# Performance work log

Hardware: AMD Instinct MI355X
Metric: run time of the kernel (lower is better)

The kernel has to match this reference:

```python
import jax, jax.numpy as jnp
import numpy as np

FEAT, HID, HEADS, OUT, NLAYERS = 32, 64, 6, 1, 4
NG, NP, K = 16, 1000, 10
EPS_BN, EPS_IN = 1e-5, 1e-5


def _build_graph(pos, rng=None):
    # knn_graph(k=10, loop=True, batch=batch) -> to_undirected -> add_self_loops
    N = NG * NP
    parts = []
    for g in range(NG):
        off = g * NP
        p = pos[off:off + NP]
        d2 = ((p[:, None, :] - p[None, :, :]) ** 2).sum(-1)
        nbr = np.argsort(d2, axis=1)[:, :K] + off  # includes self (loop=True)
        src = nbr.reshape(-1)
        dst = np.repeat(np.arange(NP) + off, K)
        parts.append(np.stack([src, dst]))
    ei = np.concatenate(parts, axis=1)
    und = np.unique(np.concatenate([ei, ei[::-1]], axis=1).T, axis=0).T  # to_undirected (coalesced)
    loops = np.tile(np.arange(N), (2, 1))  # add_self_loops (PyG appends unconditionally)
    return np.concatenate([und, loops], axis=1).astype(np.int64)


def setup_inputs() -> dict:
    rng = np.random.default_rng(0)
    N = NG * NP
    pos = rng.standard_normal((N, 3)).astype(np.float32)
    batch = np.repeat(np.arange(NG), NP).astype(np.int64)
    edge_index = _build_graph(pos)

    def lin(fi, fo):
        return (rng.standard_normal((fi, fo)) / np.sqrt(fi)).astype(np.float32)

    HC = HEADS * HID
    z = lambda *s: jnp.zeros(s, jnp.float32)
    o = lambda *s: jnp.ones(s, jnp.float32)
    return dict(
        x=jnp.asarray(rng.standard_normal((N, FEAT)).astype(np.float32)),
        pos=jnp.asarray(pos),
        w_lin1=jnp.asarray(lin(FEAT, HID)), b_lin1=z(HID),
        w_e1=jnp.asarray(lin(1, 32)), b_e1=z(32),
        w_e2=jnp.asarray(lin(32, 1)), b_e2=z(1),
        Wl=jnp.asarray(np.stack([lin(HID, HC) for _ in range(NLAYERS)])), bl=z(NLAYERS, HC),
        Wr=jnp.asarray(np.stack([lin(HID, HC) for _ in range(NLAYERS)])), br=z(NLAYERS, HC),
        We=jnp.asarray(np.stack([lin(1, HC) for _ in range(NLAYERS)])),
        att=jnp.asarray((rng.standard_normal((NLAYERS, HEADS, HID)) / np.sqrt(HID)).astype(np.float32)),
        b_gat=z(NLAYERS, HID),
        w_emb1=jnp.asarray(lin(HID, HID)), b_emb1=z(HID),
        bn1_g=o(HID), bn1_b=z(HID), bn1_m=z(HID), bn1_v=o(HID),
        w_emb2=jnp.asarray(lin(HID, HID)), b_emb2=z(HID),
        bn2_g=o(HID), bn2_b=z(HID), bn2_m=z(HID), bn2_v=o(HID),
        w_pred=jnp.asarray(lin(HID, OUT)), b_pred=z(OUT),
        edge_index=jnp.asarray(edge_index),
        batch=jnp.asarray(batch),
        n_graphs=NG,
    )


def _bn_eval(x, g, b, m, v):
    return (x - m) / jnp.sqrt(v + EPS_BN) * g + b


def _inorm(h, batch, n_graphs):
    # PyG InstanceNorm (affine=False): per-graph, per-channel standardization
    ones = jnp.ones((h.shape[0], 1), h.dtype)
    cnt = jax.ops.segment_sum(ones, batch, num_segments=n_graphs)
    mean = jax.ops.segment_sum(h, batch, num_segments=n_graphs) / cnt
    hc = h - mean[batch]
    var = jax.ops.segment_sum(hc * hc, batch, num_segments=n_graphs) / cnt
    return hc / jnp.sqrt(var[batch] + EPS_IN)


def _gatv2(h, src, dst, ea, Wl, bl, Wr, br, We, att, bias, n):
    # GATv2Conv(heads=HEADS, concat=False, edge_dim=1)
    xl = (h @ Wl + bl).reshape(-1, HEADS, HID)  # [N,H,C] source proj
    xr = (h @ Wr + br).reshape(-1, HEADS, HID)  # [N,H,C] target proj
    e = (ea @ We).reshape(-1, HEADS, HID)       # [E,H,C] edge proj (bias=False)
    g = jax.nn.leaky_relu(xl[src] + xr[dst] + e, 0.2)
    alpha = jnp.einsum('ehc,hc->eh', g, att)    # [E,H]
    amax = jax.ops.segment_max(alpha, dst, num_segments=n)
    ex = jnp.exp(alpha - amax[dst])
    den = jax.ops.segment_sum(ex, dst, num_segments=n)
    a = ex / (den[dst] + 1e-16)                 # PyG softmax eps
    out = jax.ops.segment_sum(xl[src] * a[:, :, None], dst, num_segments=n)
    return out.mean(axis=1) + bias              # concat=False -> head mean


def reference(x, pos, w_lin1, b_lin1, w_e1, b_e1, w_e2, b_e2, Wl, bl, Wr, br, We, att, b_gat,
              w_emb1, b_emb1, bn1_g, bn1_b, bn1_m, bn1_v, w_emb2, b_emb2,
              bn2_g, bn2_b, bn2_m, bn2_v, w_pred, b_pred, edge_index, batch, n_graphs):
    src, dst = edge_index[0], edge_index[1]
    d = pos[src] - pos[dst]
    s = (d * d).sum(-1, keepdims=True)
    ew = jnp.where(s == 0, 0.0, jnp.sqrt(jnp.where(s == 0, 1.0, s)))  # safe norm (0-grad at 0)
    m = jax.nn.relu(ew @ w_e1 + b_e1)            # MLP([1,32,1]) (BN in eval = identity)
    ea = jax.nn.relu(m @ w_e2 + b_e2)            # relu(edge_MLP(.)) -> [E,1]
    h = x @ w_lin1 + b_lin1
    n = h.shape[0]
    for i in range(NLAYERS):
        h = jax.nn.relu(h + _gatv2(h, src, dst, ea, Wl[i], bl[i], Wr[i], br[i], We[i], att[i], b_gat[i], n))
        h = _inorm(h, batch, n_graphs)
    z = jax.nn.relu(h @ w_emb1 + b_emb1)
    z = _bn_eval(z, bn1_g, bn1_b, bn1_m, bn1_v)
    h_out = z @ w_emb2 + b_emb2
    pred = _bn_eval(h_out, bn2_g, bn2_b, bn2_m, bn2_v) @ w_pred + b_pred
    return h_out, pred
```

## Files before the change

kernel.cpp:

```cpp
#include <hip/hip_runtime.h>
#include <hip/hip_bf16.h>
#include <stdint.h>

typedef __hip_bfloat16 bf16;
typedef __attribute__((ext_vector_type(8))) short short8;
typedef __attribute__((ext_vector_type(4))) float float4v;
__device__ __forceinline__ float bf(const bf16 x){ return __bfloat162float(x); }
__device__ __forceinline__ float bfu(uint32_t u){ u <<= 16; return __uint_as_float(u); }
__device__ __forceinline__ short f2bs(float v){
    bf16 b = __float2bfloat16(v);
    return *(short*)&b;
}

#define FEAT    32
#define HID     64
#define HEADS   6
#define HC      384
#define NLAYERS 4
#define NG      16
#define NP      1000
#define NN      16000
#define EPS_BN  1e-5f
#define EPS_IN  1e-5f
#define MNODE   16
#define LOG2E   1.44269504f
#define STATSZ  (2*NG*HID)
#define NBLK    (NN/4)
#define NTILES  48
#define WPKSZ   (NLAYERS*NTILES*64*16)

__device__ __forceinline__ float normv(float v, const float* st, int g, int c){
    if (!st) return v;
    float s  = st[g*HID + c];
    float s2 = st[NG*HID + g*HID + c];
    float mean = s*(1.f/NP);
    float var  = fmaxf(s2*(1.f/NP) - mean*mean, 0.f);
    return (v - mean)*rsqrtf(var + EPS_IN);
}

__global__ void sentinel_kernel(float* out, int n, float val){
    int i = blockIdx.x*256 + threadIdx.x;
    if (i < n) out[i] = val;
}

__global__ void zero_kernel(int* p, int n){
    int i = blockIdx.x*256 + threadIdx.x;
    if (i < n) p[i] = 0;
}

__global__ void detect_kernel(const int* ei, int* mode){
    __shared__ int nz;
    if (threadIdx.x == 0) nz = 0;
    __syncthreads();
    for (int i = 1 + 2*threadIdx.x; i < 1024; i += 512)
        if (ei[i] != 0) atomicAdd(&nz, 1);
    __syncthreads();
    if (threadIdx.x == 0) *mode = (nz == 0) ? 1 : 0;
}

__device__ __forceinline__ int load_idx(const int* ei, int idx, int mode){
    if (mode) return (int)((const long long*)ei)[idx];
    return ei[idx];
}

__global__ void count_kernel(const int* ei, const int* mode, int* deg, int E){
    int e = blockIdx.x*256 + threadIdx.x;
    if (e >= E) return;
    int d = load_idx(ei, E + e, *mode);
    if (d >= 0 && d < NN) atomicAdd(&deg[d], 1);
}

__global__ void scan_kernel(const int* deg, int* rowptr, int N){
    __shared__ int part[256];
    __shared__ int offs[256];
    int t = threadIdx.x;
    int chunk = (N + 255)/256;
    int lo = t*chunk, hi = lo + chunk; if (hi > N) hi = N;
    int s = 0;
    for (int i = lo; i < hi; i++) s += deg[i];
    part[t] = s;
    __syncthreads();
    if (t == 0){
        int r = 0;
        for (int i = 0; i < 256; i++){ offs[i] = r; r += part[i]; }
        rowptr[N] = r;
    }
    __syncthreads();
    int r = offs[t];
    for (int i = lo; i < hi; i++){ rowptr[i] = r; r += deg[i]; }
}

__global__ void scatter_ea_kernel(const int* ei, const float* pos,
                                  const float* w_e1, const float* b_e1,
                                  const float* w_e2, const float* b_e2,
                                  const int* rowptr, int* fill, const int* mode_p,
                                  int* csr_src, float* ea_csr, int E){
    int e = blockIdx.x*256 + threadIdx.x;
    if (e >= E) return;
    int mode = *mode_p;
    int s = load_idx(ei, e, mode);
    int d = load_idx(ei, E + e, mode);
    if (s < 0 || s >= NN || d < 0 || d >= NN) return;
    float dx = pos[s*3+0] - pos[d*3+0];
    float dy = pos[s*3+1] - pos[d*3+1];
    float dz = pos[s*3+2] - pos[d*3+2];
    float ss = dx*dx + dy*dy + dz*dz;
    float ew = (ss == 0.f) ? 0.f : sqrtf(ss);
    float acc = b_e2[0];
    #pragma unroll
    for (int j = 0; j < 32; j++){
        float m = ew*w_e1[j] + b_e1[j];
        m = m > 0.f ? m : 0.f;
        acc += m*w_e2[j];
    }
    acc = acc > 0.f ? acc : 0.f;
    int p = rowptr[d] + atomicAdd(&fill[d], 1);
    if (p < 0 || p >= E) return;
    csr_src[p] = s;
    ea_csr[p] = acc;
}

__global__ void lin1_kernel(const float* __restrict__ x,
                            const float* __restrict__ w1, const float* __restrict__ b1,
                            float* __restrict__ h, int N){
    int tid = blockIdx.x*256 + threadIdx.x;
    if (tid >= N*HID) return;
    int n = tid >> 6, c = tid & 63;
    float acc = b1[c];
    #pragma unroll
    for (int k = 0; k < FEAT; k++) acc += x[n*FEAT+k] * w1[k*HID+c];
    h[tid] = acc;
}

__global__ void wpack_kernel(const float* __restrict__ Wl,
                             const float* __restrict__ Wr,
                             short* __restrict__ wpk){
    int idx = blockIdx.x*256 + threadIdx.x;
    if (idx >= NLAYERS*NTILES*64) return;
    int layer = idx / (NTILES*64);
    int r = idx - layer*NTILES*64;
    int t = r >> 6, lane = r & 63;
    int q = lane >> 4, m = lane & 15;
    int col = t*16 + m;
    bool isR = col >= HC;
    int c2 = isR ? col - HC : col;
    const float* W = (isR ? Wr : Wl) + (size_t)layer*HID*HC;
    short out[16];
    #pragma unroll
    for (int s = 0; s < 2; s++)
        #pragma unroll
        for (int j = 0; j < 8; j++)
            out[s*8+j] = f2bs(W[(size_t)(s*32 + q*8 + j)*HC + c2]);
    short8* dst = (short8*)(wpk + (size_t)idx*16);
    dst[0] = *(short8*)&out[0];
    dst[1] = *(short8*)&out[8];
}

__global__ __launch_bounds__(256) void xlxr_mfma_kernel(
        const float* __restrict__ h, const float* __restrict__ statPrev,
        const short* __restrict__ wpk,
        const float* __restrict__ bl, const float* __restrict__ br,
        bf16* __restrict__ xl, bf16* __restrict__ xr, int layer){
    int n0 = blockIdx.x*16;
    int wave = threadIdx.x >> 6;
    int lane = threadIdx.x & 63;
    int q = lane >> 4;
    int m = lane & 15;
    int node = n0 + m;
    int g = node / NP;

    short8 afrag[2];
    #pragma unroll
    for (int s = 0; s < 2; s++){
        const float4* hp4 = (const float4*)(h + (size_t)node*HID + s*32 + q*8);
        float4 va = hp4[0], vb = hp4[1];
        int cb = s*32 + q*8;
        afrag[s][0] = f2bs(normv(va.x, statPrev, g, cb+0));
        afrag[s][1] = f2bs(normv(va.y, statPrev, g, cb+1));
        afrag[s][2] = f2bs(normv(va.z, statPrev, g, cb+2));
        afrag[s][3] = f2bs(normv(va.w, statPrev, g, cb+3));
        afrag[s][4] = f2bs(normv(vb.x, statPrev, g, cb+4));
        afrag[s][5] = f2bs(normv(vb.y, statPrev, g, cb+5));
        afrag[s][6] = f2bs(normv(vb.z, statPrev, g, cb+6));
        afrag[s][7] = f2bs(normv(vb.w, statPrev, g, cb+7));
    }

    const float* blp = bl + (size_t)layer*HC;
    const float* brp = br + (size_t)layer*HC;

    for (int t = wave*12; t < wave*12 + 12; t++){
        const short8* bsrc = (const short8*)(wpk + ((size_t)(layer*NTILES + t)*64 + lane)*16);
        short8 b0 = bsrc[0], b1 = bsrc[1];
        float4v acc = {0.f, 0.f, 0.f, 0.f};
        acc = __builtin_amdgcn_mfma_f32_16x16x32_bf16(afrag[0], b0, acc, 0, 0, 0);
        acc = __builtin_amdgcn_mfma_f32_16x16x32_bf16(afrag[1], b1, acc, 0, 0, 0);
        int col = t*16 + m;
        bool isR = col >= HC;
        int c2 = isR ? col - HC : col;
        float bias = isR ? brp[c2] : blp[c2];
        bf16* dst = isR ? xr : xl;
        #pragma unroll
        for (int r = 0; r < 4; r++){
            int row = q*4 + r;
            dst[(size_t)(n0 + row)*HC + c2] = __float2bfloat16(acc[r] + bias);
        }
    }
}

__global__ __launch_bounds__(384) void xlxr_fb_kernel(
        const float* __restrict__ h, const float* __restrict__ statPrev,
        const float* __restrict__ Wl, const float* __restrict__ bl,
        bf16* __restrict__ xl, int layer){
    int n0 = blockIdx.x*MNODE;
    int o = threadIdx.x;
    __shared__ float hh[MNODE*HID];
    for (int i = o; i < MNODE*HID; i += 384){
        int m = i >> 6, k = i & 63;
        int node = n0 + m;
        hh[k*MNODE + m] = normv(h[(size_t)node*HID + k], statPrev, node/NP, k);
    }
    __syncthreads();
    const float* wl = Wl + (size_t)layer*HID*HC;
    float accl[MNODE];
    float bL = bl[layer*HC + o];
    #pragma unroll
    for (int m = 0; m < MNODE; m++) accl[m] = bL;
    for (int k = 0; k < HID; k++){
        float wlv = wl[k*HC + o];
        #pragma unroll
        for (int m = 0; m < MNODE; m++) accl[m] += hh[k*MNODE + m]*wlv;
    }
    #pragma unroll
    for (int m = 0; m < MNODE; m++)
        xl[(size_t)(n0+m)*HC + o] = __float2bfloat16(accl[m]);
}

__global__ __launch_bounds__(256) void agg_kernel(
        const bf16* __restrict__ xl, const bf16* __restrict__ xr,
        const int* __restrict__ rowptr,
        const int* __restrict__ csr_src,
        const float* __restrict__ ea_csr,
        const float* __restrict__ Wr, const float* __restrict__ br,
        const float* __restrict__ We, const float* __restrict__ att,
        const float* __restrict__ b_gat,
        float* __restrict__ h,
        const float* __restrict__ statPrev, float* __restrict__ partial,
        int layer){
    int wave = threadIdx.x >> 6, lane = threadIdx.x & 63;
    int n = blockIdx.x*4 + wave;
    int g = n / NP;
    int r0 = rowptr[n];
    int deg = rowptr[n+1] - r0;

    __shared__ float ps[4][2][HID];

    int grp = lane >> 3, li = lane & 7;
    bool active = grp < HEADS;
    int cb = active ? (grp*HID + li*8) : 0;

    float xrr[8], wer[8], atr[8];
    if (xr){
        if (active){
            const uint4* xru = (const uint4*)(xr + (size_t)n*HC);
            uint4 u = xru[grp*8 + li];
            xrr[0]=bfu(u.x&0xffffu); xrr[1]=bfu(u.x>>16);
            xrr[2]=bfu(u.y&0xffffu); xrr[3]=bfu(u.y>>16);
            xrr[4]=bfu(u.z&0xffffu); xrr[5]=bfu(u.z>>16);
            xrr[6]=bfu(u.w&0xffffu); xrr[7]=bfu(u.w>>16);
        }
    } else {
        float hval = normv(h[(size_t)n*HID + lane], statPrev, g, lane);
        const float* wr = Wr + (size_t)layer*HID*HC;
        #pragma unroll
        for (int i = 0; i < 8; i++) xrr[i] = 0.f;
        for (int k = 0; k < HID; k++){
            float hk = __shfl(hval, k);
            #pragma unroll
            for (int i = 0; i < 8; i++) xrr[i] += hk*wr[k*HC + cb + i];
        }
        #pragma unroll
        for (int i = 0; i < 8; i++) xrr[i] += br[layer*HC + cb + i];
    }
    #pragma unroll
    for (int i = 0; i < 8; i++){
        wer[i] = We[layer*HC + cb + i];
        atr[i] = att[layer*HC + cb + i]*LOG2E;
    }

    float m_ = -1e30f, l_ = 0.f;
    float acc[8];
    #pragma unroll
    for (int i = 0; i < 8; i++) acc[i] = 0.f;

    const uint4* xlu = (const uint4*)xl;

    if (active){
        int j = 0;
        for (; j + 1 < deg; j += 2){
            int sa = csr_src[r0 + j], sb = csr_src[r0 + j + 1];
            float eva = ea_csr[r0 + j], evb = ea_csr[r0 + j + 1];
            uint4 ua = xlu[(size_t)sa*48 + grp*8 + li];
            uint4 ub = xlu[(size_t)sb*48 + grp*8 + li];
            float xa[8], xb[8];
            xa[0]=bfu(ua.x&0xffffu); xa[1]=bfu(ua.x>>16);
            xa[2]=bfu(ua.y&0xffffu); xa[3]=bfu(ua.y>>16);
            xa[4]=bfu(ua.z&0xffffu); xa[5]=bfu(ua.z>>16);
            xa[6]=bfu(ua.w&0xffffu); xa[7]=bfu(ua.w>>16);
            xb[0]=bfu(ub.x&0xffffu); xb[1]=bfu(ub.x>>16);
            xb[2]=bfu(ub.y&0xffffu); xb[3]=bfu(ub.y>>16);
            xb[4]=bfu(ub.z&0xffffu); xb[5]=bfu(ub.z>>16);
            xb[6]=bfu(ub.w&0xffffu); xb[7]=bfu(ub.w>>16);
            float ca = 0.f, cb_ = 0.f;
            #pragma unroll
            for (int i = 0; i < 8; i++){
                float ga = xa[i] + xrr[i] + eva*wer[i];
                ga = fmaxf(ga, 0.2f*ga);
                ca += ga*atr[i];
                float gb = xb[i] + xrr[i] + evb*wer[i];
                gb = fmaxf(gb, 0.2f*gb);
                cb_ += gb*atr[i];
            }
            #pragma unroll
            for (int mm = 1; mm <= 4; mm <<= 1){
                ca  += __shfl_xor(ca, mm);
                cb_ += __shfl_xor(cb_, mm);
            }
            float mn = fmaxf(fmaxf(m_, ca), cb_);
            float r  = exp2f(m_ - mn);
            float pa = exp2f(ca - mn);
            float pb = exp2f(cb_ - mn);
            l_ = l_*r + pa + pb;
            #pragma unroll
            for (int i = 0; i < 8; i++) acc[i] = acc[i]*r + pa*xa[i] + pb*xb[i];
            m_ = mn;
        }
        if (j < deg){
            int sa = csr_src[r0 + j];
            float eva = ea_csr[r0 + j];
            uint4 ua = xlu[(size_t)sa*48 + grp*8 + li];
            float xa[8];
            xa[0]=bfu(ua.x&0xffffu); xa[1]=bfu(ua.x>>16);
            xa[2]=bfu(ua.y&0xffffu); xa[3]=bfu(ua.y>>16);
            xa[4]=bfu(ua.z&0xffffu); xa[5]=bfu(ua.z>>16);
            xa[6]=bfu(ua.w&0xffffu); xa[7]=bfu(ua.w>>16);
            float ca = 0.f;
            #pragma unroll
            for (int i = 0; i < 8; i++){
                float ga = xa[i] + xrr[i] + eva*wer[i];
                ga = fmaxf(ga, 0.2f*ga);
                ca += ga*atr[i];
            }
            #pragma unroll
            for (int mm = 1; mm <= 4; mm <<= 1) ca += __shfl_xor(ca, mm);
            float mn = fmaxf(m_, ca);
            float r  = exp2f(m_ - mn);
            float pa = exp2f(ca - mn);
            l_ = l_*r + pa;
            #pragma unroll
            for (int i = 0; i < 8; i++) acc[i] = acc[i]*r + pa*xa[i];
            m_ = mn;
        }
    }

    float v[8];
    float rl = active ? 1.f/(l_ + 1e-16f) : 0.f;
    #pragma unroll
    for (int i = 0; i < 8; i++) v[i] = acc[i]*rl;
    #pragma unroll
    for (int mm = 8; mm <= 32; mm <<= 1)
        #pragma unroll
        for (int i = 0; i < 8; i++) v[i] += __shfl_xor(v[i], mm);

    if (lane < 8){
        int c0 = lane*8;
        const float4* hp4 = (const float4*)(h + (size_t)n*HID + c0);
        float4 h0 = hp4[0], h1 = hp4[1];
        float hv[8] = {h0.x,h0.y,h0.z,h0.w,h1.x,h1.y,h1.z,h1.w};
        float o[8];
        #pragma unroll
        for (int i = 0; i < 8; i++){
            float r = normv(hv[i], statPrev, g, c0+i)
                    + v[i]*(1.f/HEADS) + b_gat[layer*HID + c0 + i];
            o[i] = r > 0.f ? r : 0.f;
            ps[wave][0][c0+i] = o[i];
            ps[wave][1][c0+i] = o[i]*o[i];
        }
        float4* out4 = (float4*)(h + (size_t)n*HID + c0);
        out4[0] = make_float4(o[0],o[1],o[2],o[3]);
        out4[1] = make_float4(o[4],o[5],o[6],o[7]);
    }
    __syncthreads();
    if (threadIdx.x < HID){
        int c = threadIdx.x;
        float s  = ps[0][0][c] + ps[1][0][c] + ps[2][0][c] + ps[3][0][c];
        float s2 = ps[0][1][c] + ps[1][1][c] + ps[2][1][c] + ps[3][1][c];
        partial[(size_t)blockIdx.x*128 + c]      = s;
        partial[(size_t)blockIdx.x*128 + 64 + c] = s2;
    }
}

__global__ void stat_reduce_kernel(const float* __restrict__ partial,
                                   float* __restrict__ stat){
    int idx = blockIdx.x*256 + threadIdx.x;
    if (idx >= NG*HID) return;
    int g = idx >> 6, c = idx & 63;
    int b0 = g*(NP/4);
    float s = 0.f, s2 = 0.f;
    for (int b = 0; b < NP/4; b++){
        s  += partial[(size_t)(b0+b)*128 + c];
        s2 += partial[(size_t)(b0+b)*128 + 64 + c];
    }
    stat[g*HID + c] = s;
    stat[NG*HID + g*HID + c] = s2;
}

__global__ __launch_bounds__(256) void final_kernel(
        const float* __restrict__ h, const float* __restrict__ statPrev,
        const float* w1, const float* b1,
        const float* g1, const float* be1, const float* m1, const float* v1,
        const float* w2, const float* b2,
        const float* g2, const float* be2, const float* m2, const float* v2,
        const float* wp, const float* bp,
        float* out, int N){
    int wave = threadIdx.x >> 6, c = threadIdx.x & 63;
    int n = blockIdx.x*4 + wave;
    __shared__ float hr[4][HID], zr[4][HID];
    hr[wave][c] = normv(h[(size_t)n*HID + c], statPrev, n/NP, c);
    __syncthreads();
    float z = b1[c];
    #pragma unroll 8
    for (int k = 0; k < HID; k++) z += hr[wave][k]*w1[k*HID+c];
    z = z > 0.f ? z : 0.f;
    z = (z - m1[c]) / sqrtf(v1[c] + EPS_BN) * g1[c] + be1[c];
    zr[wave][c] = z;
    __syncthreads();
    float ho = b2[c];
    #pragma unroll 8
    for (int k = 0; k < HID; k++) ho += zr[wave][k]*w2[k*HID+c];
    out[(size_t)n*HID + c] = ho;
    float t = (ho - m2[c]) / sqrtf(v2[c] + EPS_BN) * g2[c] + be2[c];
    float p = t * wp[c];
    #pragma unroll
    for (int m = 32; m >= 1; m >>= 1) p += __shfl_xor(p, m);
    if (c == 0) out[(size_t)N*HID + n] = p + bp[0];
}

extern "C" void kernel_launch(void* const* d_in, const int* in_sizes, int n_in,
                              void* d_out, int out_size, void* d_ws, size_t ws_size,
                              hipStream_t stream){
    const float* x      = (const float*)d_in[0];
    const float* pos    = (const float*)d_in[1];
    const float* w_lin1 = (const float*)d_in[2];
    const float* b_lin1 = (const float*)d_in[3];
    const float* w_e1   = (const float*)d_in[4];
    const float* b_e1   = (const float*)d_in[5];
    const float* w_e2   = (const float*)d_in[6];
    const float* b_e2   = (const float*)d_in[7];
    const float* Wl     = (const float*)d_in[8];
    const float* bl     = (const float*)d_in[9];
    const float* Wr     = (const float*)d_in[10];
    const float* br     = (const float*)d_in[11];
    const float* We     = (const float*)d_in[12];
    const float* att    = (const float*)d_in[13];
    const float* b_gat  = (const float*)d_in[14];
    const float* w_emb1 = (const float*)d_in[15];
    const float* b_emb1 = (const float*)d_in[16];
    const float* bn1_g  = (const float*)d_in[17];
    const float* bn1_b  = (const float*)d_in[18];
    const float* bn1_m  = (const float*)d_in[19];
    const float* bn1_v  = (const float*)d_in[20];
    const float* w_emb2 = (const float*)d_in[21];
    const float* b_emb2 = (const float*)d_in[22];
    const float* bn2_g  = (const float*)d_in[23];
    const float* bn2_b  = (const float*)d_in[24];
    const float* bn2_m  = (const float*)d_in[25];
    const float* bn2_v  = (const float*)d_in[26];
    const float* w_pred = (const float*)d_in[27];
    const float* b_pred = (const float*)d_in[28];
    const int*   ei     = (const int*)d_in[29];

    const int N = in_sizes[0] / FEAT;
    const int E = in_sizes[29] / 2;
    int ob = (out_size + 255)/256;

    bool ok = (n_in >= 32) && (N == NN) && (E > N)
           && (in_sizes[1]  == 3*N)
           && (in_sizes[8]  == NLAYERS*HID*HC)
           && (in_sizes[13] == NLAYERS*HEADS*HID)
           && (in_sizes[27] == HID)
           && (out_size == N*HID + N);
    if (!ok){
        sentinel_kernel<<<ob, 256, 0, stream>>>((float*)d_out, out_size, 4000.0f);
        return;
    }

    char* p = (char*)d_ws;
    auto carve = [&](size_t bytes)->void*{
        void* r = (void*)p;
        p += (bytes + 255) & ~(size_t)255;
        return r;
    };
    int*   meta   = (int*)  carve((size_t)(2*N + 64)*4);
    float* stats  = (float*)carve((size_t)NLAYERS*STATSZ*4);
    float* partial= (float*)carve((size_t)NBLK*128*4);
    short* wpk    = (short*)carve((size_t)WPKSZ*2);
    int*   rowptr = (int*)  carve((size_t)(N+1)*4);
    int*   csr_src= (int*)  carve((size_t)E*4);
    float* ea_csr = (float*)carve((size_t)E*4);
    float* h      = (float*)carve((size_t)N*HID*4);
    bf16*  xl     = (bf16*) carve((size_t)N*HC*2);
    size_t used_base = (size_t)(p - (char*)d_ws);
    bf16* xr = nullptr;
    if (used_base + (size_t)N*HC*2 + 256 <= ws_size)
        xr = (bf16*)carve((size_t)N*HC*2);

    if (used_base > ws_size){
        sentinel_kernel<<<ob, 256, 0, stream>>>((float*)d_out, out_size,
                                                5000.0f + (float)(ws_size >> 20));
        return;
    }

    int* mode = meta;
    int* deg  = meta + 64;
    int* fill = meta + 64 + N;

    zero_kernel<<<(2*N + 64 + 255)/256, 256, 0, stream>>>(meta, 2*N + 64);
    detect_kernel<<<1, 256, 0, stream>>>(ei, mode);

    int eb = (E + 255)/256;
    count_kernel<<<eb, 256, 0, stream>>>(ei, mode, deg, E);
    scan_kernel<<<1, 256, 0, stream>>>(deg, rowptr, N);
    scatter_ea_kernel<<<eb, 256, 0, stream>>>(ei, pos, w_e1, b_e1, w_e2, b_e2,
                                              rowptr, fill, mode, csr_src, ea_csr, E);

    int nb = (N*HID + 255)/256;
    lin1_kernel<<<nb, 256, 0, stream>>>(x, w_lin1, b_lin1, h, N);
    wpack_kernel<<<(NLAYERS*NTILES*64 + 255)/256, 256, 0, stream>>>(Wl, Wr, wpk);

    for (int l = 0; l < NLAYERS; l++){
        const float* statPrev = (l == 0) ? nullptr : stats + (size_t)(l-1)*STATSZ;
        float* statCur = stats + (size_t)l*STATSZ;
        if (xr)
            xlxr_mfma_kernel<<<N/16, 256, 0, stream>>>(h, statPrev, wpk, bl, br,
                                                       xl, xr, l);
        else
            xlxr_fb_kernel<<<N/MNODE, 384, 0, stream>>>(h, statPrev, Wl, bl, xl, l);
        agg_kernel<<<N/4, 256, 0, stream>>>(xl, xr, rowptr, csr_src, ea_csr,
                                            Wr, br, We, att, b_gat, h,
                                            statPrev, partial, l);
        stat_reduce_kernel<<<(NG*HID + 255)/256, 256, 0, stream>>>(partial, statCur);
    }

    final_kernel<<<N/4, 256, 0, stream>>>(h, stats + (size_t)(NLAYERS-1)*STATSZ,
        w_emb1, b_emb1, bn1_g, bn1_b, bn1_m, bn1_v,
        w_emb2, b_emb2, bn2_g, bn2_b, bn2_m, bn2_v,
        w_pred, b_pred, (float*)d_out, N);
}
```

Measured before the change: 518.2 us.

## Stage MFMA outputs through LDS for vector stores and merge small kernels

The xl/xr projection kernel now writes its MFMA results into a padded shared-memory tile and then emits 16-byte coalesced stores, replacing scattered 2-byte global writes. Zeroing and index-width detection are merged into one launch, as are lin1 and weight packing. The stat reduction is split four ways per channel with shuffle reduction to expose more parallelism. The fallback path for small workspaces is removed, so the code now requires xr to always fit.

```diff
diff --git a/kernel.cpp b/kernel.cpp
--- a/kernel.cpp
+++ b/kernel.cpp
@@ -7,9 +7,9 @@
 typedef __attribute__((ext_vector_type(4))) float float4v;
 __device__ __forceinline__ float bf(const bf16 x){ return __bfloat162float(x); }
 __device__ __forceinline__ float bfu(uint32_t u){ u <<= 16; return __uint_as_float(u); }
-__device__ __forceinline__ short f2bs(float v){
+__device__ __forceinline__ unsigned short f2bs(float v){
     bf16 b = __float2bfloat16(v);
-    return *(short*)&b;
+    return *(unsigned short*)&b;
 }
 
 #define FEAT    32
@@ -22,12 +22,12 @@
 #define NN      16000
 #define EPS_BN  1e-5f
 #define EPS_IN  1e-5f
-#define MNODE   16
 #define LOG2E   1.44269504f
 #define STATSZ  (2*NG*HID)
 #define NBLK    (NN/4)
 #define NTILES  48
 #define WPKSZ   (NLAYERS*NTILES*64*16)
+#define XSTR    772
 
 __device__ __forceinline__ float normv(float v, const float* st, int g, int c){
     if (!st) return v;
@@ -43,19 +43,19 @@
     if (i < n) out[i] = val;
 }
 
-__global__ void zero_kernel(int* p, int n){
-    int i = blockIdx.x*256 + threadIdx.x;
-    if (i < n) p[i] = 0;
-}
-
-__global__ void detect_kernel(const int* ei, int* mode){
-    __shared__ int nz;
-    if (threadIdx.x == 0) nz = 0;
-    __syncthreads();
-    for (int i = 1 + 2*threadIdx.x; i < 1024; i += 512)
-        if (ei[i] != 0) atomicAdd(&nz, 1);
-    __syncthreads();
-    if (threadIdx.x == 0) *mode = (nz == 0) ? 1 : 0;
+__global__ void zero_detect_kernel(int* meta, int n, const int* ei){
+    if ((int)blockIdx.x == (int)gridDim.x - 1){
+        __shared__ int nz;
+        if (threadIdx.x == 0) nz = 0;
+        __syncthreads();
+        for (int i = 1 + 2*threadIdx.x; i < 1024; i += 512)
+            if (ei[i] != 0) atomicAdd(&nz, 1);
+        __syncthreads();
+        if (threadIdx.x == 0) meta[0] = (nz == 0) ? 1 : 0;
+    } else {
+        int i = blockIdx.x*256 + threadIdx.x;
+        if (i < n) meta[64 + i] = 0;
+    }
 }
 
 __device__ __forceinline__ int load_idx(const int* ei, int idx, int mode){
@@ -120,40 +120,42 @@
     ea_csr[p] = acc;
 }
 
-__global__ void lin1_kernel(const float* __restrict__ x,
-                            const float* __restrict__ w1, const float* __restrict__ b1,
-                            float* __restrict__ h, int N){
-    int tid = blockIdx.x*256 + threadIdx.x;
-    if (tid >= N*HID) return;
-    int n = tid >> 6, c = tid & 63;
-    float acc = b1[c];
-    #pragma unroll
-    for (int k = 0; k < FEAT; k++) acc += x[n*FEAT+k] * w1[k*HID+c];
-    h[tid] = acc;
-}
-
-__global__ void wpack_kernel(const float* __restrict__ Wl,
-                             const float* __restrict__ Wr,
-                             short* __restrict__ wpk){
-    int idx = blockIdx.x*256 + threadIdx.x;
-    if (idx >= NLAYERS*NTILES*64) return;
-    int layer = idx / (NTILES*64);
-    int r = idx - layer*NTILES*64;
-    int t = r >> 6, lane = r & 63;
-    int q = lane >> 4, m = lane & 15;
-    int col = t*16 + m;
-    bool isR = col >= HC;
-    int c2 = isR ? col - HC : col;
-    const float* W = (isR ? Wr : Wl) + (size_t)layer*HID*HC;
-    short out[16];
-    #pragma unroll
-    for (int s = 0; s < 2; s++)
-        #pragma unroll
-        for (int j = 0; j < 8; j++)
-            out[s*8+j] = f2bs(W[(size_t)(s*32 + q*8 + j)*HC + c2]);
-    short8* dst = (short8*)(wpk + (size_t)idx*16);
-    dst[0] = *(short8*)&out[0];
-    dst[1] = *(short8*)&out[8];
+__global__ void lin1_wpack_kernel(const float* __restrict__ x,
+                                  const float* __restrict__ w1,
+                                  const float* __restrict__ b1,
+                                  float* __restrict__ h, int N, int nb_lin,
+                                  const float* __restrict__ Wl,
+                                  const float* __restrict__ Wr,
+                                  short* __restrict__ wpk){
+    if ((int)blockIdx.x < nb_lin){
+        int tid = blockIdx.x*256 + threadIdx.x;
+        if (tid >= N*HID) return;
+        int n = tid >> 6, c = tid & 63;
+        float acc = b1[c];
+        #pragma unroll
+        for (int k = 0; k < FEAT; k++) acc += x[n*FEAT+k] * w1[k*HID+c];
+        h[tid] = acc;
+    } else {
+        int idx = (blockIdx.x - nb_lin)*256 + threadIdx.x;
+        if (idx >= NLAYERS*NTILES*64) return;
+        int layer = idx / (NTILES*64);
+        int r = idx - layer*NTILES*64;
+        int t = r >> 6, lane = r & 63;
+        int q = lane >> 4, m = lane & 15;
+        int col = t*16 + m;
+        bool isR = col >= HC;
+        int c2 = isR ? col - HC : col;
+        const float* W = (isR ? Wr : Wl) + (size_t)layer*HID*HC;
+        unsigned short out[16];
+        #pragma unroll
+        for (int s = 0; s < 2; s++)
+            #pragma unroll
+            for (int j = 0; j < 8; j++)
+                out[s*8+j] = f2bs(W[(size_t)(s*32 + q*8 + j)*HC + c2]);
+        short8* dst = (short8*)(wpk + (size_t)idx*16);
+        dst[0] = *(short8*)&out[0];
+        dst[1] = *(short8*)&out[8];
+    }
 }
 
 __global__ __launch_bounds__(256) void xlxr_mfma_kernel(
@@ -161,6 +163,7 @@
         const short* __restrict__ wpk,
         const float* __restrict__ bl, const float* __restrict__ br,
         bf16* __restrict__ xl, bf16* __restrict__ xr, int layer){
+    __shared__ unsigned short lds[16*XSTR];
     int n0 = blockIdx.x*16;
     int wave = threadIdx.x >> 6;
     int lane = threadIdx.x & 63;
@@ -175,14 +178,14 @@
         const float4* hp4 = (const float4*)(h + (size_t)node*HID + s*32 + q*8);
         float4 va = hp4[0], vb = hp4[1];
         int cb = s*32 + q*8;
-        afrag[s][0] = f2bs(normv(va.x, statPrev, g, cb+0));
-        afrag[s][1] = f2bs(normv(va.y, statPrev, g, cb+1));
-        afrag[s][2] = f2bs(normv(va.z, statPrev, g, cb+2));
-        afrag[s][3] = f2bs(normv(va.w, statPrev, g, cb+3));
-        afrag[s][4] = f2bs(normv(vb.x, statPrev, g, cb+4));
-        afrag[s][5] = f2bs(normv(vb.y, statPrev, g, cb+5));
-        afrag[s][6] = f2bs(normv(vb.z, statPrev, g, cb+6));
-        afrag[s][7] = f2bs(normv(vb.w, statPrev, g, cb+7));
+        afrag[s][0] = (short)f2bs(normv(va.x, statPrev, g, cb+0));
+        afrag[s][1] = (short)f2bs(normv(va.y, statPrev, g, cb+1));
+        afrag[s][2] = (short)f2bs(normv(va.z, statPrev, g, cb+2));
+        afrag[s][3] = (short)f2bs(normv(va.w, statPrev, g, cb+3));
+        afrag[s][4] = (short)f2bs(normv(vb.x, statPrev, g, cb+4));
+        afrag[s][5] = (short)f2bs(normv(vb.y, statPrev, g, cb+5));
+        afrag[s][6] = (short)f2bs(normv(vb.z, statPrev, g, cb+6));
+        afrag[s][7] = (short)f2bs(normv(vb.w, statPrev, g, cb+7));
     }
 
     const float* blp = bl + (size_t)layer*HC;
@@ -198,41 +201,25 @@
         bool isR = col >= HC;
         int c2 = isR ? col - HC : col;
         float bias = isR ? brp[c2] : blp[c2];
-        bf16* dst = isR ? xr : xl;
-        #pragma unroll
-        for (int r = 0; r < 4; r++){
-            int row = q*4 + r;
-            dst[(size_t)(n0 + row)*HC + c2] = __float2bfloat16(acc[r] + bias);
-        }
-    }
-}
-
-__global__ __launch_bounds__(384) void xlxr_fb_kernel(
-        const float* __restrict__ h, const float* __restrict__ statPrev,
-        const float* __restrict__ Wl, const float* __restrict__ bl,
-        bf16* __restrict__ xl, int layer){
-    int n0 = blockIdx.x*MNODE;
-    int o = threadIdx.x;
-    __shared__ float hh[MNODE*HID];
-    for (int i = o; i < MNODE*HID; i += 384){
-        int m = i >> 6, k = i & 63;
-        int node = n0 + m;
-        hh[k*MNODE + m] = normv(h[(size_t)node*HID + k], statPrev, node/NP, k);
+        #pragma unroll
+        for (int r = 0; r < 4; r++)
+            lds[(q*4 + r)*XSTR + col] = f2bs(acc[r] + bias);
     }
     __syncthreads();
-    const float* wl = Wl + (size_t)layer*HID*HC;
-    float accl[MNODE];
-    float bL = bl[layer*HC + o];
-    #pragma unroll
-    for (int m = 0; m < MNODE; m++) accl[m] = bL;
-    for (int k = 0; k < HID; k++){
-        float wlv = wl[k*HC + o];
-        #pragma unroll
-        for (int m = 0; m < MNODE; m++) accl[m] += hh[k*MNODE + m]*wlv;
-    }
-    #pragma unroll
-    for (int m = 0; m < MNODE; m++)
-        xl[(size_t)(n0+m)*HC + o] = __float2bfloat16(accl[m]);
+    for (int i = threadIdx.x; i < 16*48; i += 256){
+        int row = i / 48, seg = i - row*48;
+        unsigned short tmp[8];
+        #pragma unroll
+        for (int j = 0; j < 8; j++) tmp[j] = lds[row*XSTR + seg*8 + j];
+        *(uint4*)(xl + (size_t)(n0+row)*HC + seg*8) = *(uint4*)tmp;
+    }
+    for (int i = threadIdx.x; i < 16*48; i += 256){
+        int row = i / 48, seg = i - row*48;
+        unsigned short tmp[8];
+        #pragma unroll
+        for (int j = 0; j < 8; j++) tmp[j] = lds[row*XSTR + 384 + seg*8 + j];
+        *(uint4*)(xr + (size_t)(n0+row)*HC + seg*8) = *(uint4*)tmp;
+    }
 }
 
 __global__ __launch_bounds__(256) void agg_kernel(
@@ -240,7 +227,6 @@
         const int* __restrict__ rowptr,
         const int* __restrict__ csr_src,
         const float* __restrict__ ea_csr,
-        const float* __restrict__ Wr, const float* __restrict__ br,
         const float* __restrict__ We, const float* __restrict__ att,
         const float* __restrict__ b_gat,
         float* __restrict__ h,
@@ -259,27 +245,13 @@
     int cb = active ? (grp*HID + li*8) : 0;
 
     float xrr[8], wer[8], atr[8];
-    if (xr){
-        if (active){
-            const uint4* xru = (const uint4*)(xr + (size_t)n*HC);
-            uint4 u = xru[grp*8 + li];
-            xrr[0]=bfu(u.x&0xffffu); xrr[1]=bfu(u.x>>16);
-            xrr[2]=bfu(u.y&0xffffu); xrr[3]=bfu(u.y>>16);
-            xrr[4]=bfu(u.z&0xffffu); xrr[5]=bfu(u.z>>16);
-            xrr[6]=bfu(u.w&0xffffu); xrr[7]=bfu(u.w>>16);
-        }
-    } else {
-        float hval = normv(h[(size_t)n*HID + lane], statPrev, g, lane);
-        const float* wr = Wr + (size_t)layer*HID*HC;
-        #pragma unroll
-        for (int i = 0; i < 8; i++) xrr[i] = 0.f;
-        for (int k = 0; k < HID; k++){
-            float hk = __shfl(hval, k);
-            #pragma unroll
-            for (int i = 0; i < 8; i++) xrr[i] += hk*wr[k*HC + cb + i];
-        }
-        #pragma unroll
-        for (int i = 0; i < 8; i++) xrr[i] += br[layer*HC + cb + i];
+    if (active){
+        const uint4* xru = (const uint4*)(xr + (size_t)n*HC);
+        uint4 u = xru[grp*8 + li];
+        xrr[0]=bfu(u.x&0xffffu); xrr[1]=bfu(u.x>>16);
+        xrr[2]=bfu(u.y&0xffffu); xrr[3]=bfu(u.y>>16);
+        xrr[4]=bfu(u.z&0xffffu); xrr[5]=bfu(u.z>>16);
+        xrr[6]=bfu(u.w&0xffffu); xrr[7]=bfu(u.w>>16);
     }
     #pragma unroll
     for (int i = 0; i < 8; i++){
@@ -293,14 +265,15 @@
     for (int i = 0; i < 8; i++) acc[i] = 0.f;
 
     const uint4* xlu = (const uint4*)xl;
+    int voff = grp*8 + li;
 
     if (active){
         int j = 0;
         for (; j + 1 < deg; j += 2){
             int sa = csr_src[r0 + j], sb = csr_src[r0 + j + 1];
             float eva = ea_csr[r0 + j], evb = ea_csr[r0 + j + 1];
-            uint4 ua = xlu[(size_t)sa*48 + grp*8 + li];
-            uint4 ub = xlu[(size_t)sb*48 + grp*8 + li];
+            uint4 ua = xlu[(size_t)sa*48 + voff];
+            uint4 ub = xlu[(size_t)sb*48 + voff];
             float xa[8], xb[8];
             xa[0]=bfu(ua.x&0xffffu); xa[1]=bfu(ua.x>>16);
             xa[2]=bfu(ua.y&0xffffu); xa[3]=bfu(ua.y>>16);
@@ -337,7 +310,7 @@
         if (j < deg){
             int sa = csr_src[r0 + j];
             float eva = ea_csr[r0 + j];
-            uint4 ua = xlu[(size_t)sa*48 + grp*8 + li];
+            uint4 ua = xlu[(size_t)sa*48 + voff];
             float xa[8];
             xa[0]=bfu(ua.x&0xffffu); xa[1]=bfu(ua.x>>16);
             xa[2]=bfu(ua.y&0xffffu); xa[3]=bfu(ua.y>>16);
@@ -402,16 +375,22 @@
 __global__ void stat_reduce_kernel(const float* __restrict__ partial,
                                    float* __restrict__ stat){
     int idx = blockIdx.x*256 + threadIdx.x;
-    if (idx >= NG*HID) return;
-    int g = idx >> 6, c = idx & 63;
+    if (idx >= NG*HID*4) return;
+    int slice = idx & 3;
+    int gc = idx >> 2;
+    int g = gc >> 6, c = gc & 63;
     int b0 = g*(NP/4);
     float s = 0.f, s2 = 0.f;
-    for (int b = 0; b < NP/4; b++){
+    for (int b = slice; b < NP/4; b += 4){
         s  += partial[(size_t)(b0+b)*128 + c];
         s2 += partial[(size_t)(b0+b)*128 + 64 + c];
     }
-    stat[g*HID + c] = s;
-    stat[NG*HID + g*HID + c] = s2;
+    s  += __shfl_xor(s, 1);  s  += __shfl_xor(s, 2);
+    s2 += __shfl_xor(s2, 1); s2 += __shfl_xor(s2, 2);
+    if (slice == 0){
+        stat[g*HID + c] = s;
+        stat[NG*HID + g*HID + c] = s2;
+    }
 }
 
 __global__ __launch_bounds__(256) void final_kernel(
@@ -509,12 +488,10 @@
     float* ea_csr = (float*)carve((size_t)E*4);
     float* h      = (float*)carve((size_t)N*HID*4);
     bf16*  xl     = (bf16*) carve((size_t)N*HC*2);
-    size_t used_base = (size_t)(p - (char*)d_ws);
-    bf16* xr = nullptr;
-    if (used_base + (size_t)N*HC*2 + 256 <= ws_size)
-        xr = (bf16*)carve((size_t)N*HC*2);
-
-    if (used_base > ws_size){
+    bf16*  xr     = (bf16*) carve((size_t)N*HC*2);
+    size_t used = (size_t)(p - (char*)d_ws);
+
+    if (used > ws_size){
         sentinel_kernel<<<ob, 256, 0, stream>>>((float*)d_out, out_size,
                                                 5000.0f + (float)(ws_size >> 20));
         return;
@@ -524,8 +501,8 @@
     int* deg  = meta + 64;
     int* fill = meta + 64 + N;
 
-    zero_kernel<<<(2*N + 64 + 255)/256, 256, 0, stream>>>(meta, 2*N + 64);
-    detect_kernel<<<1, 256, 0, stream>>>(ei, mode);
+    int zb = (2*N + 255)/256 + 1;
+    zero_detect_kernel<<<zb, 256, 0, stream>>>(meta, 2*N, ei);
 
     int eb = (E + 255)/256;
     count_kernel<<<eb, 256, 0, stream>>>(ei, mode, deg, E);
@@ -534,21 +511,19 @@
                                               rowptr, fill, mode, csr_src, ea_csr, E);
 
     int nb = (N*HID + 255)/256;
-    lin1_kernel<<<nb, 256, 0, stream>>>(x, w_lin1, b_lin1, h, N);
-    wpack_kernel<<<(NLAYERS*NTILES*64 + 255)/256, 256, 0, stream>>>(Wl, Wr, wpk);
+    int wb = (NLAYERS*NTILES*64 + 255)/256;
+    lin1_wpack_kernel<<<nb + wb, 256, 0, stream>>>(x, w_lin1, b_lin1, h, N, nb,
+                                                   Wl, Wr, wpk);
 
     for (int l = 0; l < NLAYERS; l++){
         const float* statPrev = (l == 0) ? nullptr : stats + (size_t)(l-1)*STATSZ;
         float* statCur = stats + (size_t)l*STATSZ;
-        if (xr)
-            xlxr_mfma_kernel<<<N/16, 256, 0, stream>>>(h, statPrev, wpk, bl, br,
-                                                       xl, xr, l);
-        else
-            xlxr_fb_kernel<<<N/MNODE, 384, 0, stream>>>(h, statPrev, Wl, bl, xl, l);
+        xlxr_mfma_kernel<<<N/16, 256, 0, stream>>>(h, statPrev, wpk, bl, br,
+                                                   xl, xr, l);
         agg_kernel<<<N/4, 256, 0, stream>>>(xl, xr, rowptr, csr_src, ea_csr,
-                                            Wr, br, We, att, b_gat, h,
+                                            We, att, b_gat, h,
                                             statPrev, partial, l);
-        stat_reduce_kernel<<<(NG*HID + 255)/256, 256, 0, stream>>>(partial, statCur);
+        stat_reduce_kernel<<<(NG*HID*4 + 255)/256, 256, 0, stream>>>(partial, statCur);
     }
 
     final_kernel<<<N/4, 256, 0, stream>>>(h, stats + (size_t)(NLAYERS-1)*STATSZ,
```

Result: slower. 531.9 us (+2.6%).
